# Kernel tuning notes

Hardware: AMD Instinct MI355X
Metric: run time of the kernel (lower is better)

Reference implementation:

```python
import jax, jax.numpy as jnp
import numpy as np

PAD = 8192          # padding index == bloom_filter_dim
H1, H2 = 512, 64
B, K, L = 32, 32, 128


def prelu(x, alpha):
    return jnp.where(x >= 0, x, alpha * x)


def embedding_bag_mean(w, idx):
    # EmbeddingBag(mode='mean', padding_idx=PAD): mean over non-padding entries
    emb = w[idx]                                   # [..., L, H1]
    m = (idx != PAD)[..., None].astype(w.dtype)    # [..., L, 1]
    s = (emb * m).sum(axis=-2)
    cnt = m.sum(axis=-2)
    return jnp.where(cnt > 0, s / jnp.maximum(cnt, 1.0), 0.0)


def hidden_layers(x, W1, b1, W2, b2, a0, a1, a2):
    # PReLU -> Linear -> PReLU -> Linear -> PReLU
    h = prelu(x, a0)
    h = prelu(h @ W1 + b1, a1)
    h = prelu(h @ W2 + b2, a2)
    return h


def setup_inputs() -> dict:
    key = jax.random.key(0)
    ks = jax.random.split(key, 16)
    f = lambda i, shape: jax.random.normal(ks[i], shape, dtype=jnp.float32) * 0.05
    s = lambda v: jnp.asarray(v, dtype=jnp.float32)
    return {
        'query_bloom_filter': jax.random.randint(ks[0], (B, L), 0, PAD),
        'poi_bloom_filter': jax.random.randint(ks[1], (B, K, L), 0, PAD),
        'query_loc': jax.random.normal(ks[2], (B, 2), dtype=jnp.float32),
        'poi_loc': jax.random.normal(ks[3], (B, K, 2), dtype=jnp.float32),
        'codebook_w': f(4, (PAD + 1, H1)),
        'q_W1': f(5, (H1, H2)), 'q_b1': f(6, (H2,)),
        'q_W2': f(7, (H2, H2)), 'q_b2': f(8, (H2,)),
        'p_W1': f(9, (H1, H2)), 'p_b1': f(10, (H2,)),
        'p_W2': f(11, (H2, H2)), 'p_b2': f(12, (H2,)),
        'q_eval_w': f(13, (PAD + 1, H2)),
        'p_eval_w': f(14, (PAD + 1, H2)),
        'q_a0': s(0.25), 'q_a1': s(0.25), 'q_a2': s(0.25),
        'p_a0': s(0.25), 'p_a1': s(0.25), 'p_a2': s(0.25),
        'ind_a': s(0.25),
        'a': s(1.0), 'b': s(0.0), 'c': s(1.0), 'd': s(0.0),
    }


def reference(query_bloom_filter, poi_bloom_filter, query_loc, poi_loc,
              codebook_w, q_W1, q_b1, q_W2, q_b2, p_W1, p_b1, p_W2, p_b2,
              q_eval_w, p_eval_w, q_a0, q_a1, q_a2, p_a0, p_a1, p_a2,
              ind_a, a, b, c, d):
    # --- dense towers ---
    query_embedding = embedding_bag_mean(codebook_w, query_bloom_filter)      # [B, H1]
    query_hidden = hidden_layers(query_embedding, q_W1, q_b1, q_W2, q_b2,
                                 q_a0, q_a1, q_a2)                            # [B, H2]
    poi_embedding = embedding_bag_mean(codebook_w, poi_bloom_filter)          # [B, K, H1]
    poi_hidden = hidden_layers(poi_embedding, p_W1, p_b1, p_W2, p_b2,
                               p_a0, p_a1, p_a2)                              # [B, K, H2]

    # --- bloom-filter intersection (isin_cuda): q element present in poi set ---
    q = query_bloom_filter[:, None, :]                                        # [B, 1, L]
    p = poi_bloom_filter                                                      # [B, K, L]
    match = (q[..., :, None] == p[..., None, :]) & (p[..., None, :] != PAD)   # [B, K, L, L]
    intersection_mask = match.any(axis=-1)                                    # [B, K, L]
    intersection = jnp.where(intersection_mask, q, PAD)                       # [B, K, L]

    # --- sparse term weights via evaluator gathers + mul-sum ---
    q_cols = q_eval_w[intersection]                                           # [B, K, L, H2]
    p_cols = p_eval_w[intersection]                                           # [B, K, L, H2]
    q_sw = prelu(jnp.einsum('bh,bklh->bkl', query_hidden, q_cols), ind_a) + 1.0
    p_sw = prelu(jnp.einsum('bkh,bklh->bkl', poi_hidden, p_cols), ind_a) + 1.0

    text_sim = jnp.where(intersection_mask, q_sw * p_sw, 0.0).sum(axis=-1)    # [B, K]

    # --- location similarity ---
    dist = jnp.sqrt(((query_loc[:, None, :] - poi_loc) ** 2).sum(axis=-1))    # [B, K]
    dist_sim = -jnp.log(dist + 1.0)

    # --- text-sim normalization + relevance ---
    max_sim = text_sim.max(axis=-1, keepdims=True)
    text_sim = (2.0 * text_sim - max_sim) / (max_sim + 1e-6)
    relevance_score = (c - jax.nn.sigmoid(a * text_sim + b)) * (dist_sim - d)
    return relevance_score
```

## Files before the change

kernel.cpp:

```cpp
#include <hip/hip_runtime.h>
#include <hip/hip_bf16.h>

#define PAD_V 8192
#define H1 512
#define H2 64
#define B_SZ 32
#define K_SZ 32
#define L_SZ 128
#define EMB_BLOCKS (B_SZ + B_SZ * K_SZ)
#define ISECT_BLOCKS ((B_SZ * K_SZ) / 4)

__global__ __launch_bounds__(512, 8) void front_kernel(
    const int* __restrict__ qbf, const int* __restrict__ pbf,
    const float* __restrict__ codebook,
    const float* __restrict__ qW1, const float* __restrict__ qb1,
    const float* __restrict__ qW2, const float* __restrict__ qb2,
    const float* __restrict__ pW1, const float* __restrict__ pb1,
    const float* __restrict__ pW2, const float* __restrict__ pb2,
    const float* __restrict__ qa0p, const float* __restrict__ qa1p, const float* __restrict__ qa2p,
    const float* __restrict__ pa0p, const float* __restrict__ pa1p, const float* __restrict__ pa2p,
    float* __restrict__ qh_out, float* __restrict__ ph_out,
    int* __restrict__ nh_ws, int* __restrict__ hits_ws)
{
    const int tid = threadIdx.x;

    if (blockIdx.x >= EMB_BLOCKS) {
        __shared__ unsigned int bm4[4][256];
        __shared__ int s_nh4[4];
        __shared__ int s_hit4[4][L_SZ];

        const int pair0 = (blockIdx.x - EMB_BLOCKS) * 4;
        const int sub = tid >> 7;
        const int t   = tid & 127;
        const int pair = pair0 + sub;
        const int b = pair >> 5;

        bm4[sub][t] = 0u; bm4[sub][t + 128] = 0u;
        if (t == 0) s_nh4[sub] = 0;
        __syncthreads();

        int pv = pbf[pair * L_SZ + t];
        if ((unsigned)pv < (unsigned)PAD_V)
            atomicOr(&bm4[sub][pv >> 5], 1u << (pv & 31));
        __syncthreads();

        int v = qbf[b * L_SZ + t];
        bool hit = ((unsigned)v < (unsigned)PAD_V) &&
                   ((bm4[sub][v >> 5] >> (v & 31)) & 1u);
        if (hit) {
            int pos = atomicAdd(&s_nh4[sub], 1);
            s_hit4[sub][pos] = v;
        }
        __syncthreads();

        if (t == 0) nh_ws[pair] = s_nh4[sub];
        if (t < s_nh4[sub]) hits_ws[pair * L_SZ + t] = s_hit4[sub][t];
        return;
    }

    const bool is_q = (blockIdx.x < B_SZ);
    const int* idx_base;
    int bag;
    const float *W1, *b1, *W2, *b2;
    float a0, a1, a2;
    float* out;
    if (is_q) {
        idx_base = qbf; bag = blockIdx.x;
        W1 = qW1; b1 = qb1; W2 = qW2; b2 = qb2;
        a0 = *qa0p; a1 = *qa1p; a2 = *qa2p;
        out = qh_out;
    } else {
        idx_base = pbf; bag = blockIdx.x - B_SZ;
        W1 = pW1; b1 = pb1; W2 = pW2; b2 = pb2;
        a0 = *pa0p; a1 = *pa1p; a2 = *pa2p;
        out = ph_out;
    }

    __shared__ int   s_idx[L_SZ];
    __shared__ int   s_cntp[2];
    __shared__ float s_red[3][L_SZ][4];
    __shared__ float s_x[H1];
    __shared__ float s_p1[32][H2];
    __shared__ float s_h1[H2];

    if (tid < L_SZ) s_idx[tid] = idx_base[bag * L_SZ + tid];
    __syncthreads();

    if (tid < L_SZ) {
        unsigned long long bal = __ballot(s_idx[tid] != PAD_V);
        if ((tid & 63) == 0) s_cntp[tid >> 6] = __popcll(bal);
    }

    const int g = tid & 127;
    const int q = tid >> 7;
    const float4* cb4 = (const float4*)codebook;
    float ax = 0.f, ay = 0.f, az = 0.f, aw = 0.f;
    #pragma unroll 8
    for (int l = 0; l < 32; l++) {
        int v = s_idx[q * 32 + l];
        float m = (v != PAD_V) ? 1.0f : 0.0f;
        float4 r = cb4[(size_t)v * 128 + g];
        ax = fmaf(m, r.x, ax);
        ay = fmaf(m, r.y, ay);
        az = fmaf(m, r.z, az);
        aw = fmaf(m, r.w, aw);
    }
    if (q != 0) {
        s_red[q - 1][g][0] = ax; s_red[q - 1][g][1] = ay;
        s_red[q - 1][g][2] = az; s_red[q - 1][g][3] = aw;
    }
    __syncthreads();
    if (q == 0) {
        int cnt = s_cntp[0] + s_cntp[1];
        float inv = (cnt > 0) ? 1.0f / (float)cnt : 0.0f;
        float e0 = (ax + s_red[0][g][0] + s_red[1][g][0] + s_red[2][g][0]) * inv;
        float e1 = (ay + s_red[0][g][1] + s_red[1][g][1] + s_red[2][g][1]) * inv;
        float e2 = (az + s_red[0][g][2] + s_red[1][g][2] + s_red[2][g][2]) * inv;
        float e3 = (aw + s_red[0][g][3] + s_red[1][g][3] + s_red[2][g][3]) * inv;
        s_x[4 * g + 0] = (e0 >= 0.f) ? e0 : a0 * e0;
        s_x[4 * g + 1] = (e1 >= 0.f) ? e1 : a0 * e1;
        s_x[4 * g + 2] = (e2 >= 0.f) ? e2 : a0 * e2;
        s_x[4 * g + 3] = (e3 >= 0.f) ? e3 : a0 * e3;
    }
    __syncthreads();

    const int j4 = tid & 15;
    const int ch = tid >> 4;
    const float4* W1v = (const float4*)W1;
    {
        const int i0 = ch * 16;
        float sx = 0.f, sy = 0.f, sz = 0.f, sw = 0.f;
        #pragma unroll
        for (int i = 0; i < 16; i++) {
            float x = s_x[i0 + i];
            float4 w = W1v[(size_t)(i0 + i) * 16 + j4];
            sx = fmaf(x, w.x, sx);
            sy = fmaf(x, w.y, sy);
            sz = fmaf(x, w.z, sz);
            sw = fmaf(x, w.w, sw);
        }
        s_p1[ch][4 * j4 + 0] = sx;
        s_p1[ch][4 * j4 + 1] = sy;
        s_p1[ch][4 * j4 + 2] = sz;
        s_p1[ch][4 * j4 + 3] = sw;
    }
    __syncthreads();
    if (tid < H2) {
        float s = b1[tid];
        #pragma unroll
        for (int r = 0; r < 32; r++) s += s_p1[r][tid];
        s_h1[tid] = (s >= 0.f) ? s : a1 * s;
    }
    __syncthreads();

    const float4* W2v = (const float4*)W2;
    {
        const int i0 = ch * 2;
        float sx = 0.f, sy = 0.f, sz = 0.f, sw = 0.f;
        #pragma unroll
        for (int i = 0; i < 2; i++) {
            float x = s_h1[i0 + i];
            float4 w = W2v[(size_t)(i0 + i) * 16 + j4];
            sx = fmaf(x, w.x, sx);
            sy = fmaf(x, w.y, sy);
            sz = fmaf(x, w.z, sz);
            sw = fmaf(x, w.w, sw);
        }
        s_p1[ch][4 * j4 + 0] = sx;
        s_p1[ch][4 * j4 + 1] = sy;
        s_p1[ch][4 * j4 + 2] = sz;
        s_p1[ch][4 * j4 + 3] = sw;
    }
    __syncthreads();
    if (tid < H2) {
        float s = b2[tid];
        #pragma unroll
        for (int r = 0; r < 32; r++) s += s_p1[r][tid];
        s = (s >= 0.f) ? s : a2 * s;
        out[bag * H2 + tid] = s;
    }
}

__global__ __launch_bounds__(64) void text_sim_kernel(
    const float* __restrict__ q_eval, const float* __restrict__ p_eval,
    const float* __restrict__ qh_ws, const float* __restrict__ ph_ws,
    const int* __restrict__ nh_ws, const int* __restrict__ hits_ws,
    const float* __restrict__ ind_ap,
    float* __restrict__ text_out)
{
    const int blk = blockIdx.x;
    const int b    = blk >> 5;
    const int lane = threadIdx.x;

    const float qh = qh_ws[b * H2 + lane];
    const float ph = ph_ws[blk * H2 + lane];
    const int   nh = nh_ws[blk];
    const float ind_a = *ind_ap;

    float local = 0.f;
    for (int hh = 0; hh < nh; hh++) {
        int v = hits_ws[blk * L_SZ + hh];
        float qd = qh * q_eval[(size_t)v * H2 + lane];
        float pd = ph * p_eval[(size_t)v * H2 + lane];
        #pragma unroll
        for (int m = 1; m < 64; m <<= 1) {
            qd += __shfl_xor(qd, m);
            pd += __shfl_xor(pd, m);
        }
        qd = (qd >= 0.f) ? qd : ind_a * qd;
        pd = (pd >= 0.f) ? pd : ind_a * pd;
        local += (qd + 1.f) * (pd + 1.f);
    }
    if (lane == 0) text_out[blk] = local;
}

__global__ __launch_bounds__(64) void epilogue_kernel(
    const float* __restrict__ text_ws,
    const float* __restrict__ qloc, const float* __restrict__ ploc,
    const float* __restrict__ ap, const float* __restrict__ bp,
    const float* __restrict__ cp, const float* __restrict__ dp,
    float* __restrict__ out)
{
    const int b = blockIdx.x;
    const int t = threadIdx.x;
    const int kk = t & 31;

    float ts_raw = text_ws[b * K_SZ + kk];
    float mx = ts_raw;
    #pragma unroll
    for (int m = 1; m < 32; m <<= 1) mx = fmaxf(mx, __shfl_xor(mx, m));

    float qx = qloc[b * 2], qy = qloc[b * 2 + 1];
    float px = ploc[(b * K_SZ + kk) * 2];
    float py = ploc[(b * K_SZ + kk) * 2 + 1];
    float dx = qx - px, dy = qy - py;
    float dist = sqrtf(dx * dx + dy * dy);
    float ds = -logf(dist + 1.0f);

    float ts = (2.0f * ts_raw - mx) / (mx + 1e-6f);
    float A = *ap, Bb = *bp, C = *cp, D = *dp;
    float sig = 1.0f / (1.0f + expf(-(A * ts + Bb)));
    if (t < 32) out[b * K_SZ + kk] = (C - sig) * (ds - D);
}

extern "C" void kernel_launch(void* const* d_in, const int* in_sizes, int n_in,
                              void* d_out, int out_size, void* d_ws, size_t ws_size,
                              hipStream_t stream) {
    const int*   qbf      = (const int*)d_in[0];
    const int*   pbf      = (const int*)d_in[1];
    const float* qloc     = (const float*)d_in[2];
    const float* ploc     = (const float*)d_in[3];
    const float* codebook = (const float*)d_in[4];
    const float* qW1      = (const float*)d_in[5];
    const float* qb1      = (const float*)d_in[6];
    const float* qW2      = (const float*)d_in[7];
    const float* qb2      = (const float*)d_in[8];
    const float* pW1      = (const float*)d_in[9];
    const float* pb1      = (const float*)d_in[10];
    const float* pW2      = (const float*)d_in[11];
    const float* pb2      = (const float*)d_in[12];
    const float* q_eval   = (const float*)d_in[13];
    const float* p_eval   = (const float*)d_in[14];
    const float* qa0      = (const float*)d_in[15];
    const float* qa1      = (const float*)d_in[16];
    const float* qa2      = (const float*)d_in[17];
    const float* pa0      = (const float*)d_in[18];
    const float* pa1      = (const float*)d_in[19];
    const float* pa2      = (const float*)d_in[20];
    const float* ind_a    = (const float*)d_in[21];
    const float* a        = (const float*)d_in[22];
    const float* bsc      = (const float*)d_in[23];
    const float* c        = (const float*)d_in[24];
    const float* d        = (const float*)d_in[25];

    float* qh   = (float*)d_ws;
    float* ph   = qh + B_SZ * H2;
    float* text = ph + B_SZ * K_SZ * H2;
    int*   nh   = (int*)(text + B_SZ * K_SZ);
    int*   hits = nh + B_SZ * K_SZ;

    front_kernel<<<EMB_BLOCKS + ISECT_BLOCKS, 512, 0, stream>>>(
        qbf, pbf, codebook,
        qW1, qb1, qW2, qb2, pW1, pb1, pW2, pb2,
        qa0, qa1, qa2, pa0, pa1, pa2,
        qh, ph, nh, hits);

    text_sim_kernel<<<B_SZ * K_SZ, 64, 0, stream>>>(
        q_eval, p_eval, qh, ph, nh, hits, ind_a, text);

    epilogue_kernel<<<B_SZ, 64, 0, stream>>>(
        text, qloc, ploc, a, bsc, c, d, (float*)d_out);
}
```

Baseline: 155.0 us.

## Batch four bags per block in front kernel and fuse text-sim with epilogue

The embedding/MLP part of the front kernel now handles four bags per 512-thread block. Each 128-thread group reduces one full bag, and the W1/W2 weight loads are shared across the four bags, which cuts block count and weight reloads. The text-similarity and epilogue kernels are merged into one 32-block kernel with 16 waves per block, which removes a launch and the workspace round trip. The trade-off is less parallelism: the front kernel has fewer blocks with longer per-thread gather loops, and the fused similarity kernel runs only 32 blocks, which may underfill the GPU.

Measured after the change: 167.1 us. 1.08x slower.

```diff
diff --git a/kernel.cpp b/kernel.cpp
--- a/kernel.cpp
+++ b/kernel.cpp
@@ -1,5 +1,4 @@
 #include <hip/hip_runtime.h>
-#include <hip/hip_bf16.h>
 
 #define PAD_V 8192
 #define H1 512
@@ -7,10 +6,10 @@
 #define B_SZ 32
 #define K_SZ 32
 #define L_SZ 128
-#define EMB_BLOCKS (B_SZ + B_SZ * K_SZ)
+#define EMB4_BLOCKS ((B_SZ + B_SZ * K_SZ) / 4)
 #define ISECT_BLOCKS ((B_SZ * K_SZ) / 4)
 
-__global__ __launch_bounds__(512, 8) void front_kernel(
+__global__ __launch_bounds__(512, 6) void front_kernel(
     const int* __restrict__ qbf, const int* __restrict__ pbf,
     const float* __restrict__ codebook,
     const float* __restrict__ qW1, const float* __restrict__ qb1,
@@ -24,12 +23,12 @@
 {
     const int tid = threadIdx.x;
 
-    if (blockIdx.x >= EMB_BLOCKS) {
+    if (blockIdx.x >= EMB4_BLOCKS) {
         __shared__ unsigned int bm4[4][256];
         __shared__ int s_nh4[4];
         __shared__ int s_hit4[4][L_SZ];
 
-        const int pair0 = (blockIdx.x - EMB_BLOCKS) * 4;
+        const int pair0 = (blockIdx.x - EMB4_BLOCKS) * 4;
         const int sub = tid >> 7;
         const int t   = tid & 127;
         const int pair = pair0 + sub;
@@ -58,189 +57,212 @@
         return;
     }
 
-    const bool is_q = (blockIdx.x < B_SZ);
+    __shared__ int   s_idx[4][L_SZ];
+    __shared__ int   s_cntw[8];
+    __shared__ float s_x[4][H1];
+    __shared__ float s_p1[4][32][H2];
+    __shared__ float s_h1[4][H2];
+
+    const bool is_q = (blockIdx.x < (B_SZ / 4));
     const int* idx_base;
-    int bag;
+    int bag0;
     const float *W1, *b1, *W2, *b2;
     float a0, a1, a2;
     float* out;
     if (is_q) {
-        idx_base = qbf; bag = blockIdx.x;
+        idx_base = qbf; bag0 = blockIdx.x * 4;
         W1 = qW1; b1 = qb1; W2 = qW2; b2 = qb2;
         a0 = *qa0p; a1 = *qa1p; a2 = *qa2p;
         out = qh_out;
     } else {
-        idx_base = pbf; bag = blockIdx.x - B_SZ;
+        idx_base = pbf; bag0 = (blockIdx.x - (B_SZ / 4)) * 4;
         W1 = pW1; b1 = pb1; W2 = pW2; b2 = pb2;
         a0 = *pa0p; a1 = *pa1p; a2 = *pa2p;
         out = ph_out;
     }
 
-    __shared__ int   s_idx[L_SZ];
-    __shared__ int   s_cntp[2];
-    __shared__ float s_red[3][L_SZ][4];
-    __shared__ float s_x[H1];
-    __shared__ float s_p1[32][H2];
-    __shared__ float s_h1[H2];
-
-    if (tid < L_SZ) s_idx[tid] = idx_base[bag * L_SZ + tid];
-    __syncthreads();
-
-    if (tid < L_SZ) {
-        unsigned long long bal = __ballot(s_idx[tid] != PAD_V);
-        if ((tid & 63) == 0) s_cntp[tid >> 6] = __popcll(bal);
-    }
-
-    const int g = tid & 127;
-    const int q = tid >> 7;
-    const float4* cb4 = (const float4*)codebook;
-    float ax = 0.f, ay = 0.f, az = 0.f, aw = 0.f;
-    #pragma unroll 8
-    for (int l = 0; l < 32; l++) {
-        int v = s_idx[q * 32 + l];
-        float m = (v != PAD_V) ? 1.0f : 0.0f;
-        float4 r = cb4[(size_t)v * 128 + g];
-        ax = fmaf(m, r.x, ax);
-        ay = fmaf(m, r.y, ay);
-        az = fmaf(m, r.z, az);
-        aw = fmaf(m, r.w, aw);
-    }
-    if (q != 0) {
-        s_red[q - 1][g][0] = ax; s_red[q - 1][g][1] = ay;
-        s_red[q - 1][g][2] = az; s_red[q - 1][g][3] = aw;
-    }
-    __syncthreads();
-    if (q == 0) {
-        int cnt = s_cntp[0] + s_cntp[1];
+    const int sub = tid >> 7;
+    const int t   = tid & 127;
+
+    {
+        int v = idx_base[(bag0 + sub) * L_SZ + t];
+        s_idx[sub][t] = v;
+        unsigned long long bal = __ballot(v != PAD_V);
+        if ((tid & 63) == 0) s_cntw[tid >> 6] = __popcll(bal);
+    }
+    __syncthreads();
+
+    {
+        const float4* cb4 = (const float4*)codebook;
+        float ax = 0.f, ay = 0.f, az = 0.f, aw = 0.f;
+        #pragma unroll 8
+        for (int l = 0; l < L_SZ; l++) {
+            int u = s_idx[sub][l];
+            float m = (u != PAD_V) ? 1.0f : 0.0f;
+            float4 r = cb4[(size_t)u * 128 + t];
+            ax = fmaf(m, r.x, ax);
+            ay = fmaf(m, r.y, ay);
+            az = fmaf(m, r.z, az);
+            aw = fmaf(m, r.w, aw);
+        }
+        int cnt = s_cntw[2 * sub] + s_cntw[2 * sub + 1];
         float inv = (cnt > 0) ? 1.0f / (float)cnt : 0.0f;
-        float e0 = (ax + s_red[0][g][0] + s_red[1][g][0] + s_red[2][g][0]) * inv;
-        float e1 = (ay + s_red[0][g][1] + s_red[1][g][1] + s_red[2][g][1]) * inv;
-        float e2 = (az + s_red[0][g][2] + s_red[1][g][2] + s_red[2][g][2]) * inv;
-        float e3 = (aw + s_red[0][g][3] + s_red[1][g][3] + s_red[2][g][3]) * inv;
-        s_x[4 * g + 0] = (e0 >= 0.f) ? e0 : a0 * e0;
-        s_x[4 * g + 1] = (e1 >= 0.f) ? e1 : a0 * e1;
-        s_x[4 * g + 2] = (e2 >= 0.f) ? e2 : a0 * e2;
-        s_x[4 * g + 3] = (e3 >= 0.f) ? e3 : a0 * e3;
+        float e0 = ax * inv, e1 = ay * inv, e2 = az * inv, e3 = aw * inv;
+        s_x[sub][4 * t + 0] = (e0 >= 0.f) ? e0 : a0 * e0;
+        s_x[sub][4 * t + 1] = (e1 >= 0.f) ? e1 : a0 * e1;
+        s_x[sub][4 * t + 2] = (e2 >= 0.f) ? e2 : a0 * e2;
+        s_x[sub][4 * t + 3] = (e3 >= 0.f) ? e3 : a0 * e3;
     }
     __syncthreads();
 
     const int j4 = tid & 15;
     const int ch = tid >> 4;
-    const float4* W1v = (const float4*)W1;
+
     {
+        const float4* W1v = (const float4*)W1;
         const int i0 = ch * 16;
-        float sx = 0.f, sy = 0.f, sz = 0.f, sw = 0.f;
+        float4 A0 = make_float4(0.f,0.f,0.f,0.f);
+        float4 A1 = make_float4(0.f,0.f,0.f,0.f);
+        float4 A2 = make_float4(0.f,0.f,0.f,0.f);
+        float4 A3 = make_float4(0.f,0.f,0.f,0.f);
+        #pragma unroll 8
+        for (int i = 0; i < 16; i++) {
+            float4 w = W1v[(size_t)(i0 + i) * 16 + j4];
+            float x0 = s_x[0][i0 + i];
+            float x1 = s_x[1][i0 + i];
+            float x2 = s_x[2][i0 + i];
+            float x3 = s_x[3][i0 + i];
+            A0.x = fmaf(x0, w.x, A0.x); A0.y = fmaf(x0, w.y, A0.y);
+            A0.z = fmaf(x0, w.z, A0.z); A0.w = fmaf(x0, w.w, A0.w);
+            A1.x = fmaf(x1, w.x, A1.x); A1.y = fmaf(x1, w.y, A1.y);
+            A1.z = fmaf(x1, w.z, A1.z); A1.w = fmaf(x1, w.w, A1.w);
+            A2.x = fmaf(x2, w.x, A2.x); A2.y = fmaf(x2, w.y, A2.y);
+            A2.z = fmaf(x2, w.z, A2.z); A2.w = fmaf(x2, w.w, A2.w);
+            A3.x = fmaf(x3, w.x, A3.x); A3.y = fmaf(x3, w.y, A3.y);
+            A3.z = fmaf(x3, w.z, A3.z); A3.w = fmaf(x3, w.w, A3.w);
+        }
+        s_p1[0][ch][4*j4+0] = A0.x; s_p1[0][ch][4*j4+1] = A0.y;
+        s_p1[0][ch][4*j4+2] = A0.z; s_p1[0][ch][4*j4+3] = A0.w;
+        s_p1[1][ch][4*j4+0] = A1.x; s_p1[1][ch][4*j4+1] = A1.y;
+        s_p1[1][ch][4*j4+2] = A1.z; s_p1[1][ch][4*j4+3] = A1.w;
+        s_p1[2][ch][4*j4+0] = A2.x; s_p1[2][ch][4*j4+1] = A2.y;
+        s_p1[2][ch][4*j4+2] = A2.z; s_p1[2][ch][4*j4+3] = A2.w;
+        s_p1[3][ch][4*j4+0] = A3.x; s_p1[3][ch][4*j4+1] = A3.y;
+        s_p1[3][ch][4*j4+2] = A3.z; s_p1[3][ch][4*j4+3] = A3.w;
+    }
+    __syncthreads();
+    if (tid < 256) {
+        const int bg = tid >> 6, col = tid & 63;
+        float s = b1[col];
         #pragma unroll
-        for (int i = 0; i < 16; i++) {
-            float x = s_x[i0 + i];
-            float4 w = W1v[(size_t)(i0 + i) * 16 + j4];
-            sx = fmaf(x, w.x, sx);
-            sy = fmaf(x, w.y, sy);
-            sz = fmaf(x, w.z, sz);
-            sw = fmaf(x, w.w, sw);
-        }
-        s_p1[ch][4 * j4 + 0] = sx;
-        s_p1[ch][4 * j4 + 1] = sy;
-        s_p1[ch][4 * j4 + 2] = sz;
-        s_p1[ch][4 * j4 + 3] = sw;
-    }
-    __syncthreads();
-    if (tid < H2) {
-        float s = b1[tid];
-        #pragma unroll
-        for (int r = 0; r < 32; r++) s += s_p1[r][tid];
-        s_h1[tid] = (s >= 0.f) ? s : a1 * s;
-    }
-    __syncthreads();
-
-    const float4* W2v = (const float4*)W2;
+        for (int r = 0; r < 32; r++) s += s_p1[bg][r][col];
+        s_h1[bg][col] = (s >= 0.f) ? s : a1 * s;
+    }
+    __syncthreads();
+
     {
+        const float4* W2v = (const float4*)W2;
         const int i0 = ch * 2;
-        float sx = 0.f, sy = 0.f, sz = 0.f, sw = 0.f;
+        float4 A0 = make_float4(0.f,0.f,0.f,0.f);
+        float4 A1 = make_float4(0.f,0.f,0.f,0.f);
+        float4 A2 = make_float4(0.f,0.f,0.f,0.f);
+        float4 A3 = make_float4(0.f,0.f,0.f,0.f);
         #pragma unroll
         for (int i = 0; i < 2; i++) {
-            float x = s_h1[i0 + i];
             float4 w = W2v[(size_t)(i0 + i) * 16 + j4];
-            sx = fmaf(x, w.x, sx);
-            sy = fmaf(x, w.y, sy);
-            sz = fmaf(x, w.z, sz);
-            sw = fmaf(x, w.w, sw);
-        }
-        s_p1[ch][4 * j4 + 0] = sx;
-        s_p1[ch][4 * j4 + 1] = sy;
-        s_p1[ch][4 * j4 + 2] = sz;
-        s_p1[ch][4 * j4 + 3] = sw;
-    }
-    __syncthreads();
-    if (tid < H2) {
-        float s = b2[tid];
+            float x0 = s_h1[0][i0 + i];
+            float x1 = s_h1[1][i0 + i];
+            float x2 = s_h1[2][i0 + i];
+            float x3 = s_h1[3][i0 + i];
+            A0.x = fmaf(x0, w.x, A0.x); A0.y = fmaf(x0, w.y, A0.y);
+            A0.z = fmaf(x0, w.z, A0.z); A0.w = fmaf(x0, w.w, A0.w);
+            A1.x = fmaf(x1, w.x, A1.x); A1.y = fmaf(x1, w.y, A1.y);
+            A1.z = fmaf(x1, w.z, A1.z); A1.w = fmaf(x1, w.w, A1.w);
+            A2.x = fmaf(x2, w.x, A2.x); A2.y = fmaf(x2, w.y, A2.y);
+            A2.z = fmaf(x2, w.z, A2.z); A2.w = fmaf(x2, w.w, A2.w);
+            A3.x = fmaf(x3, w.x, A3.x); A3.y = fmaf(x3, w.y, A3.y);
+            A3.z = fmaf(x3, w.z, A3.z); A3.w = fmaf(x3, w.w, A3.w);
+        }
+        s_p1[0][ch][4*j4+0] = A0.x; s_p1[0][ch][4*j4+1] = A0.y;
+        s_p1[0][ch][4*j4+2] = A0.z; s_p1[0][ch][4*j4+3] = A0.w;
+        s_p1[1][ch][4*j4+0] = A1.x; s_p1[1][ch][4*j4+1] = A1.y;
+        s_p1[1][ch][4*j4+2] = A1.z; s_p1[1][ch][4*j4+3] = A1.w;
+        s_p1[2][ch][4*j4+0] = A2.x; s_p1[2][ch][4*j4+1] = A2.y;
+        s_p1[2][ch][4*j4+2] = A2.z; s_p1[2][ch][4*j4+3] = A2.w;
+        s_p1[3][ch][4*j4+0] = A3.x; s_p1[3][ch][4*j4+1] = A3.y;
+        s_p1[3][ch][4*j4+2] = A3.z; s_p1[3][ch][4*j4+3] = A3.w;
+    }
+    __syncthreads();
+    if (tid < 256) {
+        const int bg = tid >> 6, col = tid & 63;
+        float s = b2[col];
         #pragma unroll
-        for (int r = 0; r < 32; r++) s += s_p1[r][tid];
+        for (int r = 0; r < 32; r++) s += s_p1[bg][r][col];
         s = (s >= 0.f) ? s : a2 * s;
-        out[bag * H2 + tid] = s;
+        out[(bag0 + bg) * H2 + col] = s;
     }
 }
 
-__global__ __launch_bounds__(64) void text_sim_kernel(
+__global__ __launch_bounds__(1024) void sim_epilogue_kernel(
     const float* __restrict__ q_eval, const float* __restrict__ p_eval,
     const float* __restrict__ qh_ws, const float* __restrict__ ph_ws,
     const int* __restrict__ nh_ws, const int* __restrict__ hits_ws,
     const float* __restrict__ ind_ap,
-    float* __restrict__ text_out)
-{
-    const int blk = blockIdx.x;
-    const int b    = blk >> 5;
-    const int lane = threadIdx.x;
-
-    const float qh = qh_ws[b * H2 + lane];
-    const float ph = ph_ws[blk * H2 + lane];
-    const int   nh = nh_ws[blk];
-    const float ind_a = *ind_ap;
-
-    float local = 0.f;
-    for (int hh = 0; hh < nh; hh++) {
-        int v = hits_ws[blk * L_SZ + hh];
-        float qd = qh * q_eval[(size_t)v * H2 + lane];
-        float pd = ph * p_eval[(size_t)v * H2 + lane];
-        #pragma unroll
-        for (int m = 1; m < 64; m <<= 1) {
-            qd += __shfl_xor(qd, m);
-            pd += __shfl_xor(pd, m);
-        }
-        qd = (qd >= 0.f) ? qd : ind_a * qd;
-        pd = (pd >= 0.f) ? pd : ind_a * pd;
-        local += (qd + 1.f) * (pd + 1.f);
-    }
-    if (lane == 0) text_out[blk] = local;
-}
-
-__global__ __launch_bounds__(64) void epilogue_kernel(
-    const float* __restrict__ text_ws,
     const float* __restrict__ qloc, const float* __restrict__ ploc,
     const float* __restrict__ ap, const float* __restrict__ bp,
     const float* __restrict__ cp, const float* __restrict__ dp,
     float* __restrict__ out)
 {
-    const int b = blockIdx.x;
-    const int t = threadIdx.x;
-    const int kk = t & 31;
-
-    float ts_raw = text_ws[b * K_SZ + kk];
-    float mx = ts_raw;
-    #pragma unroll
-    for (int m = 1; m < 32; m <<= 1) mx = fmaxf(mx, __shfl_xor(mx, m));
-
-    float qx = qloc[b * 2], qy = qloc[b * 2 + 1];
-    float px = ploc[(b * K_SZ + kk) * 2];
-    float py = ploc[(b * K_SZ + kk) * 2 + 1];
-    float dx = qx - px, dy = qy - py;
-    float dist = sqrtf(dx * dx + dy * dy);
-    float ds = -logf(dist + 1.0f);
-
-    float ts = (2.0f * ts_raw - mx) / (mx + 1e-6f);
-    float A = *ap, Bb = *bp, C = *cp, D = *dp;
-    float sig = 1.0f / (1.0f + expf(-(A * ts + Bb)));
-    if (t < 32) out[b * K_SZ + kk] = (C - sig) * (ds - D);
+    const int b    = blockIdx.x;
+    const int tid  = threadIdx.x;
+    const int wave = tid >> 6;
+    const int lane = tid & 63;
+    __shared__ float s_text[K_SZ];
+
+    const float ind_a = *ind_ap;
+    const float qh = qh_ws[b * H2 + lane];
+
+    for (int kk = wave; kk < K_SZ; kk += 16) {
+        const int blk = b * K_SZ + kk;
+        const float ph = ph_ws[blk * H2 + lane];
+        const int   nh = nh_ws[blk];
+        float local = 0.f;
+        for (int hh = 0; hh < nh; hh++) {
+            int v = hits_ws[blk * L_SZ + hh];
+            float qd = qh * q_eval[(size_t)v * H2 + lane];
+            float pd = ph * p_eval[(size_t)v * H2 + lane];
+            #pragma unroll
+            for (int m = 1; m < 64; m <<= 1) {
+                qd += __shfl_xor(qd, m);
+                pd += __shfl_xor(pd, m);
+            }
+            qd = (qd >= 0.f) ? qd : ind_a * qd;
+            pd = (pd >= 0.f) ? pd : ind_a * pd;
+            local += (qd + 1.f) * (pd + 1.f);
+        }
+        if (lane == 0) s_text[kk] = local;
+    }
+    __syncthreads();
+
+    if (tid < K_SZ) {
+        const int kk = tid;
+        float ts_raw = s_text[kk];
+        float mx = ts_raw;
+        #pragma unroll
+        for (int m = 1; m < 32; m <<= 1) mx = fmaxf(mx, __shfl_xor(mx, m));
+
+        float qx = qloc[b * 2], qy = qloc[b * 2 + 1];
+        float px = ploc[(b * K_SZ + kk) * 2];
+        float py = ploc[(b * K_SZ + kk) * 2 + 1];
+        float dx = qx - px, dy = qy - py;
+        float dist = sqrtf(dx * dx + dy * dy);
+        float ds = -logf(dist + 1.0f);
+
+        float ts = (2.0f * ts_raw - mx) / (mx + 1e-6f);
+        float A = *ap, Bb = *bp, C = *cp, D = *dp;
+        float sig = 1.0f / (1.0f + expf(-(A * ts + Bb)));
+        out[b * K_SZ + kk] = (C - sig) * (ds - D);
+    }
 }
 
 extern "C" void kernel_launch(void* const* d_in, const int* in_sizes, int n_in,
@@ -275,19 +297,16 @@
 
     float* qh   = (float*)d_ws;
     float* ph   = qh + B_SZ * H2;
-    float* text = ph + B_SZ * K_SZ * H2;
-    int*   nh   = (int*)(text + B_SZ * K_SZ);
+    int*   nh   = (int*)(ph + B_SZ * K_SZ * H2);
     int*   hits = nh + B_SZ * K_SZ;
 
-    front_kernel<<<EMB_BLOCKS + ISECT_BLOCKS, 512, 0, stream>>>(
+    front_kernel<<<EMB4_BLOCKS + ISECT_BLOCKS, 512, 0, stream>>>(
         qbf, pbf, codebook,
         qW1, qb1, qW2, qb2, pW1, pb1, pW2, pb2,
         qa0, qa1, qa2, pa0, pa1, pa2,
         qh, ph, nh, hits);
 
-    text_sim_kernel<<<B_SZ * K_SZ, 64, 0, stream>>>(
-        q_eval, p_eval, qh, ph, nh, hits, ind_a, text);
-
-    epilogue_kernel<<<B_SZ, 64, 0, stream>>>(
-        text, qloc, ploc, a, bsc, c, d, (float*)d_out);
+    sim_epilogue_kernel<<<B_SZ, 1024, 0, stream>>>(
+        q_eval, p_eval, qh, ph, nh, hits, ind_a,
+        qloc, ploc, a, bsc, c, d, (float*)d_out);
 }
```
